# Optimization experiments

Measured on AMD Instinct MI355X. Metric: run time of the kernel, lower is better.

The kernel has to match this reference:

```python
import jax, jax.numpy as jnp
import numpy as np

L, B, N, D = 512, 8, 32, 256
GH, AH = 128, 64  # gate hidden, attn hidden


def setup_inputs() -> dict:
    key = jax.random.key(0)
    ks = jax.random.split(key, 11)
    s = lambda fan_in: 1.0 / np.sqrt(fan_in)
    return {
        "vert_feat": jax.random.normal(ks[0], (L, B, N, D), jnp.float32),
        "horiz_feat": jax.random.normal(ks[1], (L, B, N, D), jnp.float32),
        "mask_BNL": jax.random.bernoulli(ks[2], 0.5, (B, N, L)),
        "gw1": jax.random.uniform(ks[3], (GH, 2 * D), jnp.float32, -s(2 * D), s(2 * D)),
        "gb1": jax.random.uniform(ks[4], (GH,), jnp.float32, -s(2 * D), s(2 * D)),
        "gw2": jax.random.uniform(ks[5], (1, GH), jnp.float32, -s(GH), s(GH)),
        "gb2": jax.random.uniform(ks[6], (1,), jnp.float32, -s(GH), s(GH)),
        "aw1": jax.random.uniform(ks[7], (AH, D), jnp.float32, -s(D), s(D)),
        "ab1": jax.random.uniform(ks[8], (AH,), jnp.float32, -s(D), s(D)),
        "aw2": jax.random.uniform(ks[9], (1, AH), jnp.float32, -s(AH), s(AH)),
        "ab2": jax.random.uniform(ks[10], (1,), jnp.float32, -s(AH), s(AH)),
    }


def reference(vert_feat, horiz_feat, mask_BNL, gw1, gb1, gw2, gb2, aw1, ab1, aw2, ab2):
    # gate MLP on concat features: [L,B,N,2D] -> [L,B,N,1]
    comb = jnp.concatenate([vert_feat, horiz_feat], axis=-1)
    h = jax.nn.relu(comb @ gw1.T + gb1)
    gate = jax.nn.sigmoid(h @ gw2.T + gb2)  # [L,B,N,1]
    per_msg = gate * vert_feat + (1.0 - gate) * horiz_feat  # [L,B,N,D]
    # scorer MLP -> logits [L,B,N]
    a = jnp.tanh(per_msg @ aw1.T + ab1)
    logits = (a @ aw2.T + ab2)[..., 0]  # [L,B,N]
    logits_BLN = jnp.transpose(logits, (1, 0, 2))  # [B,L,N]
    mask_BLN = jnp.transpose(mask_BNL, (0, 2, 1))  # [B,L,N]
    logits_BLN = jnp.where(mask_BLN, logits_BLN, -jnp.inf)
    attn = jax.nn.softmax(logits_BLN, axis=-1)
    attn = jnp.nan_to_num(attn, nan=0.0)  # rows fully masked -> 0
    # weighted sum over messages: per_msg as [B,L,N,D]
    fused_BLD = jnp.einsum("bln,lbnd->bld", attn, per_msg)
    fused = jnp.transpose(fused_BLD, (1, 0, 2))  # [L,B,D]
    return fused, per_msg, attn
```

## Files before the change

### kernel.cpp

```cpp
#include <hip/hip_runtime.h>
#include <hip/hip_bf16.h>
#include <math.h>

#define LL 512
#define BB 8
#define NN 32
#define DD 256
#define GH 128
#define AH 64

#define PA 520

typedef short short8 __attribute__((ext_vector_type(8)));
typedef float f32x4  __attribute__((ext_vector_type(4)));

__device__ __forceinline__ float bf2f(unsigned short u) {
  return __uint_as_float(((unsigned int)u) << 16);
}
__device__ __forceinline__ unsigned short f2bf(float f) {
  union { __hip_bfloat16 h; unsigned short u; } cv;
  cv.h = __float2bfloat16(f);
  return cv.u;
}

extern "C" __global__ void wconv(const float* __restrict__ gw1,
                                 const float* __restrict__ aw1,
                                 unsigned short* __restrict__ ws)
{
  int o = blockIdx.x * 256 + threadIdx.x;
  if (o < 65536) {
    int kb = o >> 12, r = o & 4095, j = r >> 5, ko = r & 31;
    ws[o] = f2bf(gw1[j * 512 + kb * 32 + ko]);
  } else {
    int o2 = o - 65536;
    int kb = o2 >> 11, j = (o2 >> 5) & 63, ko = o2 & 31;
    ws[o] = f2bf(aw1[j * 256 + kb * 32 + ko]);
  }
}

extern "C" __global__ __launch_bounds__(256, 4)
void dynfusion_kernel(const float* __restrict__ vert,
                      const float* __restrict__ horiz,
                      const int*   __restrict__ mask,
                      const float* __restrict__ gb1,
                      const float* __restrict__ gw2,
                      const float* __restrict__ gb2,
                      const float* __restrict__ ab1,
                      const float* __restrict__ aw2,
                      const float* __restrict__ ab2,
                      const unsigned short* __restrict__ ws,
                      float* __restrict__ out)
{
  __shared__ __align__(16) unsigned short sA[NN * PA];
  __shared__ float sPart[NN][2];
  __shared__ float sGb1R[GH], sGw2R[GH];
  __shared__ float sAb1R[AH], sAw2R[AH];
  __shared__ float sGate[NN], sAttn[NN], sScal[2];

  const int t  = threadIdx.x;
  const int lb = blockIdx.x;
  const int l  = lb >> 3;
  const int b  = lb & 7;
  const size_t msgBase = (size_t)lb * NN * DD;

  const int lane = t & 63;
  const int w    = t >> 6;
  const int lr   = lane & 15;
  const int lg   = lane >> 4;
  const int mt   = w & 1;
  const int ns   = (w >> 1) << 6;
  const int js   = (w >> 1) << 5;
  const int aoff = (mt * 16 + lr) * PA;

  const unsigned short* __restrict__ gw1t = ws;
  const unsigned short* __restrict__ aw1t = ws + 65536;

  float* __restrict__ outF  = out;
  float* __restrict__ outPM = out + 1048576;
  float* __restrict__ outAT = out + 34603008;

  int mval = 0;
  if (t < NN) mval = mask[((size_t)b * NN + t) * LL + l];

  if (t < GH) { sGb1R[t] = gb1[t]; sGw2R[t] = gw2[t]; }
  if (t < AH) { sAb1R[t] = ab1[t]; sAw2R[t] = aw2[t]; }
  if (t == 0) { sScal[0] = gb2[0]; sScal[1] = ab2[0]; }

#pragma unroll
  for (int i = 0; i < 16; ++i) {
    int idx4 = i * 256 + t;
    int n  = idx4 >> 7;
    int c4 = (idx4 & 127) << 2;
    const float* src = (c4 < DD) ? (vert  + msgBase + n * DD + c4)
                                 : (horiz + msgBase + n * DD + (c4 - DD));
    float4 v4 = *reinterpret_cast<const float4*>(src);
    ushort4 pk;
    pk.x = f2bf(v4.x); pk.y = f2bf(v4.y); pk.z = f2bf(v4.z); pk.w = f2bf(v4.w);
    *reinterpret_cast<ushort4*>(&sA[n * PA + c4]) = pk;
  }
  __syncthreads();

  f32x4 acc1[4] = {};
  {
    const unsigned short* bgp = gw1t + (ns + lr) * 32 + lg * 8;
#pragma unroll
    for (int ks = 0; ks < 16; ++ks) {
      short8 af = *reinterpret_cast<const short8*>(&sA[aoff + ks * 32 + lg * 8]);
#pragma unroll
      for (int nt = 0; nt < 4; ++nt) {
        short8 bf = *reinterpret_cast<const short8*>(bgp + ks * 4096 + nt * 512);
        acc1[nt] = __builtin_amdgcn_mfma_f32_16x16x32_bf16(af, bf, acc1[nt], 0, 0, 0);
      }
    }
  }

  {
    float p[4] = {0.f, 0.f, 0.f, 0.f};
#pragma unroll
    for (int nt = 0; nt < 4; ++nt) {
      int j = ns + nt * 16 + lr;
      float bj = sGb1R[j], wj = sGw2R[j];
#pragma unroll
      for (int r = 0; r < 4; ++r) {
        float hv = fmaxf(acc1[nt][r] + bj, 0.0f);
        p[r] += hv * wj;
      }
    }
#pragma unroll
    for (int msk = 1; msk <= 8; msk <<= 1)
#pragma unroll
      for (int r = 0; r < 4; ++r) p[r] += __shfl_xor(p[r], msk);
    if (lr == 0) {
#pragma unroll
      for (int r = 0; r < 4; ++r) sPart[mt * 16 + lg * 4 + r][w >> 1] = p[r];
    }
  }
  __syncthreads();
  if (t < NN) {
    float sv = sScal[0] + sPart[t][0] + sPart[t][1];
    sGate[t] = 1.0f / (1.0f + __expf(-sv));
  }
  __syncthreads();

#pragma unroll
  for (int i = 0; i < 8; ++i) {
    int idx4 = i * 256 + t;
    int n  = idx4 >> 6;
    int d0 = (idx4 & 63) << 2;
    float g = sGate[n];
    ushort4 vq = *reinterpret_cast<const ushort4*>(&sA[n * PA + d0]);
    ushort4 hq = *reinterpret_cast<const ushort4*>(&sA[n * PA + DD + d0]);
    float4 pr;
    pr.x = bf2f(hq.x) + g * (bf2f(vq.x) - bf2f(hq.x));
    pr.y = bf2f(hq.y) + g * (bf2f(vq.y) - bf2f(hq.y));
    pr.z = bf2f(hq.z) + g * (bf2f(vq.z) - bf2f(hq.z));
    pr.w = bf2f(hq.w) + g * (bf2f(vq.w) - bf2f(hq.w));
    ushort4 pq;
    pq.x = f2bf(pr.x); pq.y = f2bf(pr.y); pq.z = f2bf(pr.z); pq.w = f2bf(pr.w);
    *reinterpret_cast<ushort4*>(&sA[n * PA + d0]) = pq;
    *reinterpret_cast<float4*>(outPM + msgBase + n * DD + d0) = pr;
  }
  __syncthreads();

  f32x4 acc2[2] = {};
  {
    const unsigned short* bap = aw1t + (js + lr) * 32 + lg * 8;
#pragma unroll
    for (int ks = 0; ks < 8; ++ks) {
      short8 af = *reinterpret_cast<const short8*>(&sA[aoff + ks * 32 + lg * 8]);
#pragma unroll
      for (int q = 0; q < 2; ++q) {
        short8 bf = *reinterpret_cast<const short8*>(bap + ks * 2048 + q * 512);
        acc2[q] = __builtin_amdgcn_mfma_f32_16x16x32_bf16(af, bf, acc2[q], 0, 0, 0);
      }
    }
  }

  {
    float p[4] = {0.f, 0.f, 0.f, 0.f};
#pragma unroll
    for (int q = 0; q < 2; ++q) {
      int j = js + q * 16 + lr;
      float bj = sAb1R[j], wj = sAw2R[j];
#pragma unroll
      for (int r = 0; r < 4; ++r) {
        float av = tanhf(acc2[q][r] + bj);
        p[r] += av * wj;
      }
    }
#pragma unroll
    for (int msk = 1; msk <= 8; msk <<= 1)
#pragma unroll
      for (int r = 0; r < 4; ++r) p[r] += __shfl_xor(p[r], msk);
    if (lr == 0) {
#pragma unroll
      for (int r = 0; r < 4; ++r) sPart[mt * 16 + lg * 4 + r][w >> 1] = p[r];
    }
  }
  __syncthreads();

  if (t < 64) {
    float logit = -INFINITY;
    bool valid = false;
    if (t < 32) {
      float sv = sScal[1] + sPart[t][0] + sPart[t][1];
      valid = (mval != 0);
      logit = valid ? sv : -INFINITY;
    }
    float m = logit;
#pragma unroll
    for (int off = 32; off >= 1; off >>= 1) m = fmaxf(m, __shfl_xor(m, off));
    float e = (valid && m > -INFINITY) ? __expf(logit - m) : 0.0f;
    float ssum = e;
#pragma unroll
    for (int off = 32; off >= 1; off >>= 1) ssum += __shfl_xor(ssum, off);
    float at = (ssum > 0.0f) ? (e / ssum) : 0.0f;
    if (t < 32) {
      sAttn[t] = at;
      outAT[((size_t)b * LL + l) * NN + t] = at;
    }
  }
  __syncthreads();

  {
    int d = t;
    float f = 0.0f;
#pragma unroll
    for (int n = 0; n < NN; ++n) f += sAttn[n] * bf2f(sA[n * PA + d]);
    outF[(size_t)lb * DD + d] = f;
  }
}

extern "C" void kernel_launch(void* const* d_in, const int* in_sizes, int n_in,
                              void* d_out, int out_size, void* d_ws, size_t ws_size,
                              hipStream_t stream) {
  wconv<<<dim3(320), dim3(256), 0, stream>>>(
      (const float*)d_in[3],
      (const float*)d_in[7],
      (unsigned short*)d_ws);

  dynfusion_kernel<<<dim3(LL * BB), dim3(256), 0, stream>>>(
      (const float*)d_in[0],
      (const float*)d_in[1],
      (const int*)d_in[2],
      (const float*)d_in[4],
      (const float*)d_in[5],
      (const float*)d_in[6],
      (const float*)d_in[8],
      (const float*)d_in[9],
      (const float*)d_in[10],
      (const unsigned short*)d_ws,
      (float*)d_out);
}
```

Before: 389.2 us.

## Process four (l,b) groups per block with register-prefetched next inputs

Each block now loops over four consecutive (l,b) groups. The next group's vert/horiz tile and mask are loaded into registers while the current group's MFMA and softmax stages run, so global-load latency overlaps compute. The change also swaps __syncthreads for a barrier that waits only on LDS counters, and raises wave priority around the MFMA loops. The cost is 64 extra float registers per thread for the prefetch, which may cut occupancy, plus a grid four times smaller.

```diff
diff --git a/kernel.cpp b/kernel.cpp
--- a/kernel.cpp
+++ b/kernel.cpp
@@ -10,6 +10,8 @@
 #define AH 64
 
 #define PA 520
+#define NPAIR 4
+#define NBLK (LL * BB / NPAIR)
 
 typedef short short8 __attribute__((ext_vector_type(8)));
 typedef float f32x4  __attribute__((ext_vector_type(4)));
@@ -21,6 +23,12 @@
   union { __hip_bfloat16 h; unsigned short u; } cv;
   cv.h = __float2bfloat16(f);
   return cv.u;
+}
+
+__device__ __forceinline__ void barrier_lds() {
+  asm volatile("s_waitcnt lgkmcnt(0)" ::: "memory");
+  __builtin_amdgcn_s_barrier();
+  __builtin_amdgcn_sched_barrier(0);
 }
 
 extern "C" __global__ void wconv(const float* __restrict__ gw1,
@@ -57,11 +65,8 @@
   __shared__ float sAb1R[AH], sAw2R[AH];
   __shared__ float sGate[NN], sAttn[NN], sScal[2];
 
-  const int t  = threadIdx.x;
-  const int lb = blockIdx.x;
-  const int l  = lb >> 3;
-  const int b  = lb & 7;
-  const size_t msgBase = (size_t)lb * NN * DD;
+  const int t   = threadIdx.x;
+  const int bid = blockIdx.x;
 
   const int lane = t & 63;
   const int w    = t >> 6;
@@ -79,155 +84,202 @@
   float* __restrict__ outPM = out + 1048576;
   float* __restrict__ outAT = out + 34603008;
 
-  int mval = 0;
-  if (t < NN) mval = mask[((size_t)b * NN + t) * LL + l];
-
   if (t < GH) { sGb1R[t] = gb1[t]; sGw2R[t] = gw2[t]; }
   if (t < AH) { sAb1R[t] = ab1[t]; sAw2R[t] = aw2[t]; }
   if (t == 0) { sScal[0] = gb2[0]; sScal[1] = ab2[0]; }
 
-#pragma unroll
-  for (int i = 0; i < 16; ++i) {
-    int idx4 = i * 256 + t;
-    int n  = idx4 >> 7;
-    int c4 = (idx4 & 127) << 2;
-    const float* src = (c4 < DD) ? (vert  + msgBase + n * DD + c4)
-                                 : (horiz + msgBase + n * DD + (c4 - DD));
-    float4 v4 = *reinterpret_cast<const float4*>(src);
-    ushort4 pk;
-    pk.x = f2bf(v4.x); pk.y = f2bf(v4.y); pk.z = f2bf(v4.z); pk.w = f2bf(v4.w);
-    *reinterpret_cast<ushort4*>(&sA[n * PA + c4]) = pk;
+  float4 pf[16];
+  {
+    const size_t base0 = (size_t)(bid * NPAIR) * NN * DD;
+#pragma unroll
+    for (int i = 0; i < 16; ++i) {
+      int idx4 = i * 256 + t;
+      int n  = idx4 >> 7;
+      int c4 = (idx4 & 127) << 2;
+      const float* src = (c4 < DD) ? (vert  + base0 + n * DD + c4)
+                                   : (horiz + base0 + n * DD + (c4 - DD));
+      pf[i] = *reinterpret_cast<const float4*>(src);
+    }
   }
-  __syncthreads();
-
-  f32x4 acc1[4] = {};
+  int mval = 0;
   {
-    const unsigned short* bgp = gw1t + (ns + lr) * 32 + lg * 8;
-#pragma unroll
-    for (int ks = 0; ks < 16; ++ks) {
-      short8 af = *reinterpret_cast<const short8*>(&sA[aoff + ks * 32 + lg * 8]);
+    int lb0 = bid * NPAIR;
+    if (t < NN) mval = mask[((size_t)(lb0 & 7) * NN + t) * LL + (lb0 >> 3)];
+  }
+
+#pragma unroll 1
+  for (int p = 0; p < NPAIR; ++p) {
+    const int lb = bid * NPAIR + p;
+    const int l  = lb >> 3;
+    const int b  = lb & 7;
+    const size_t msgBase = (size_t)lb * NN * DD;
+
+    __syncthreads();
+
+#pragma unroll
+    for (int i = 0; i < 16; ++i) {
+      int idx4 = i * 256 + t;
+      int n  = idx4 >> 7;
+      int c4 = (idx4 & 127) << 2;
+      ushort4 pk;
+      pk.x = f2bf(pf[i].x); pk.y = f2bf(pf[i].y);
+      pk.z = f2bf(pf[i].z); pk.w = f2bf(pf[i].w);
+      *reinterpret_cast<ushort4*>(&sA[n * PA + c4]) = pk;
+    }
+
+    int mnext = 0;
+    if (p + 1 < NPAIR) {
+      const size_t baseN = msgBase + (size_t)NN * DD;
+#pragma unroll
+      for (int i = 0; i < 16; ++i) {
+        int idx4 = i * 256 + t;
+        int n  = idx4 >> 7;
+        int c4 = (idx4 & 127) << 2;
+        const float* src = (c4 < DD) ? (vert  + baseN + n * DD + c4)
+                                     : (horiz + baseN + n * DD + (c4 - DD));
+        pf[i] = *reinterpret_cast<const float4*>(src);
+      }
+      int lb2 = lb + 1;
+      if (t < NN) mnext = mask[((size_t)(lb2 & 7) * NN + t) * LL + (lb2 >> 3)];
+    }
+
+    barrier_lds();
+
+    f32x4 acc1[4] = {};
+    {
+      const unsigned short* bgp = gw1t + (ns + lr) * 32 + lg * 8;
+      __builtin_amdgcn_s_setprio(1);
+#pragma unroll
+      for (int ks = 0; ks < 16; ++ks) {
+        short8 af = *reinterpret_cast<const short8*>(&sA[aoff + ks * 32 + lg * 8]);
+#pragma unroll
+        for (int nt = 0; nt < 4; ++nt) {
+          short8 bf = *reinterpret_cast<const short8*>(bgp + ks * 4096 + nt * 512);
+          acc1[nt] = __builtin_amdgcn_mfma_f32_16x16x32_bf16(af, bf, acc1[nt], 0, 0, 0);
+        }
+      }
+      __builtin_amdgcn_s_setprio(0);
+    }
+
+    {
+      float pr[4] = {0.f, 0.f, 0.f, 0.f};
 #pragma unroll
       for (int nt = 0; nt < 4; ++nt) {
-        short8 bf = *reinterpret_cast<const short8*>(bgp + ks * 4096 + nt * 512);
-        acc1[nt] = __builtin_amdgcn_mfma_f32_16x16x32_bf16(af, bf, acc1[nt], 0, 0, 0);
-      }
-    }
-  }
-
-  {
-    float p[4] = {0.f, 0.f, 0.f, 0.f};
-#pragma unroll
-    for (int nt = 0; nt < 4; ++nt) {
-      int j = ns + nt * 16 + lr;
-      float bj = sGb1R[j], wj = sGw2R[j];
-#pragma unroll
-      for (int r = 0; r < 4; ++r) {
-        float hv = fmaxf(acc1[nt][r] + bj, 0.0f);
-        p[r] += hv * wj;
-      }
-    }
-#pragma unroll
-    for (int msk = 1; msk <= 8; msk <<= 1)
-#pragma unroll
-      for (int r = 0; r < 4; ++r) p[r] += __shfl_xor(p[r], msk);
-    if (lr == 0) {
-#pragma unroll
-      for (int r = 0; r < 4; ++r) sPart[mt * 16 + lg * 4 + r][w >> 1] = p[r];
-    }
-  }
-  __syncthreads();
-  if (t < NN) {
-    float sv = sScal[0] + sPart[t][0] + sPart[t][1];
-    sGate[t] = 1.0f / (1.0f + __expf(-sv));
-  }
-  __syncthreads();
-
-#pragma unroll
-  for (int i = 0; i < 8; ++i) {
-    int idx4 = i * 256 + t;
-    int n  = idx4 >> 6;
-    int d0 = (idx4 & 63) << 2;
-    float g = sGate[n];
-    ushort4 vq = *reinterpret_cast<const ushort4*>(&sA[n * PA + d0]);
-    ushort4 hq = *reinterpret_cast<const ushort4*>(&sA[n * PA + DD + d0]);
-    float4 pr;
-    pr.x = bf2f(hq.x) + g * (bf2f(vq.x) - bf2f(hq.x));
-    pr.y = bf2f(hq.y) + g * (bf2f(vq.y) - bf2f(hq.y));
-    pr.z = bf2f(hq.z) + g * (bf2f(vq.z) - bf2f(hq.z));
-    pr.w = bf2f(hq.w) + g * (bf2f(vq.w) - bf2f(hq.w));
-    ushort4 pq;
-    pq.x = f2bf(pr.x); pq.y = f2bf(pr.y); pq.z = f2bf(pr.z); pq.w = f2bf(pr.w);
-    *reinterpret_cast<ushort4*>(&sA[n * PA + d0]) = pq;
-    *reinterpret_cast<float4*>(outPM + msgBase + n * DD + d0) = pr;
-  }
-  __syncthreads();
-
-  f32x4 acc2[2] = {};
-  {
-    const unsigned short* bap = aw1t + (js + lr) * 32 + lg * 8;
-#pragma unroll
-    for (int ks = 0; ks < 8; ++ks) {
-      short8 af = *reinterpret_cast<const short8*>(&sA[aoff + ks * 32 + lg * 8]);
+        int j = ns + nt * 16 + lr;
+        float bj = sGb1R[j], wj = sGw2R[j];
+#pragma unroll
+        for (int r = 0; r < 4; ++r) {
+          float hv = fmaxf(acc1[nt][r] + bj, 0.0f);
+          pr[r] += hv * wj;
+        }
+      }
+#pragma unroll
+      for (int msk = 1; msk <= 8; msk <<= 1)
+#pragma unroll
+        for (int r = 0; r < 4; ++r) pr[r] += __shfl_xor(pr[r], msk);
+      if (lr == 0) {
+#pragma unroll
+        for (int r = 0; r < 4; ++r) sPart[mt * 16 + lg * 4 + r][w >> 1] = pr[r];
+      }
+    }
+    barrier_lds();
+    if (t < NN) {
+      float sv = sScal[0] + sPart[t][0] + sPart[t][1];
+      sGate[t] = 1.0f / (1.0f + __expf(-sv));
+    }
+    barrier_lds();
+
+#pragma unroll
+    for (int i = 0; i < 8; ++i) {
+      int idx4 = i * 256 + t;
+      int n  = idx4 >> 6;
+      int d0 = (idx4 & 63) << 2;
+      float g = sGate[n];
+      ushort4 vq = *reinterpret_cast<const ushort4*>(&sA[n * PA + d0]);
+      ushort4 hq = *reinterpret_cast<const ushort4*>(&sA[n * PA + DD + d0]);
+      float4 prv;
+      prv.x = bf2f(hq.x) + g * (bf2f(vq.x) - bf2f(hq.x));
+      prv.y = bf2f(hq.y) + g * (bf2f(vq.y) - bf2f(hq.y));
+      prv.z = bf2f(hq.z) + g * (bf2f(vq.z) - bf2f(hq.z));
+      prv.w = bf2f(hq.w) + g * (bf2f(vq.w) - bf2f(hq.w));
+      ushort4 pq;
+      pq.x = f2bf(prv.x); pq.y = f2bf(prv.y); pq.z = f2bf(prv.z); pq.w = f2bf(prv.w);
+      *reinterpret_cast<ushort4*>(&sA[n * PA + d0]) = pq;
+      *reinterpret_cast<float4*>(outPM + msgBase + n * DD + d0) = prv;
+    }
+    barrier_lds();
+
+    f32x4 acc2[2] = {};
+    {
+      const unsigned short* bap = aw1t + (js + lr) * 32 + lg * 8;
+      __builtin_amdgcn_s_setprio(1);
+#pragma unroll
+      for (int ks = 0; ks < 8; ++ks) {
+        short8 af = *reinterpret_cast<const short8*>(&sA[aoff + ks * 32 + lg * 8]);
+#pragma unroll
+        for (int q = 0; q < 2; ++q) {
+          short8 bf = *reinterpret_cast<const short8*>(bap + ks * 2048 + q * 512);
+          acc2[q] = __builtin_amdgcn_mfma_f32_16x16x32_bf16(af, bf, acc2[q], 0, 0, 0);
+        }
+      }
+      __builtin_amdgcn_s_setprio(0);
+    }
+
+    {
+      float pr[4] = {0.f, 0.f, 0.f, 0.f};
 #pragma unroll
       for (int q = 0; q < 2; ++q) {
-        short8 bf = *reinterpret_cast<const short8*>(bap + ks * 2048 + q * 512);
-        acc2[q] = __builtin_amdgcn_mfma_f32_16x16x32_bf16(af, bf, acc2[q], 0, 0, 0);
-      }
-    }
-  }
-
-  {
-    float p[4] = {0.f, 0.f, 0.f, 0.f};
-#pragma unroll
-    for (int q = 0; q < 2; ++q) {
-      int j = js + q * 16 + lr;
-      float bj = sAb1R[j], wj = sAw2R[j];
-#pragma unroll
-      for (int r = 0; r < 4; ++r) {
-        float av = tanhf(acc2[q][r] + bj);
-        p[r] += av * wj;
-      }
-    }
-#pragma unroll
-    for (int msk = 1; msk <= 8; msk <<= 1)
-#pragma unroll
-      for (int r = 0; r < 4; ++r) p[r] += __shfl_xor(p[r], msk);
-    if (lr == 0) {
-#pragma unroll
-      for (int r = 0; r < 4; ++r) sPart[mt * 16 + lg * 4 + r][w >> 1] = p[r];
-    }
-  }
-  __syncthreads();
-
-  if (t < 64) {
-    float logit = -INFINITY;
-    bool valid = false;
-    if (t < 32) {
-      float sv = sScal[1] + sPart[t][0] + sPart[t][1];
-      valid = (mval != 0);
-      logit = valid ? sv : -INFINITY;
-    }
-    float m = logit;
-#pragma unroll
-    for (int off = 32; off >= 1; off >>= 1) m = fmaxf(m, __shfl_xor(m, off));
-    float e = (valid && m > -INFINITY) ? __expf(logit - m) : 0.0f;
-    float ssum = e;
-#pragma unroll
-    for (int off = 32; off >= 1; off >>= 1) ssum += __shfl_xor(ssum, off);
-    float at = (ssum > 0.0f) ? (e / ssum) : 0.0f;
-    if (t < 32) {
-      sAttn[t] = at;
-      outAT[((size_t)b * LL + l) * NN + t] = at;
-    }
-  }
-  __syncthreads();
-
-  {
-    int d = t;
-    float f = 0.0f;
-#pragma unroll
-    for (int n = 0; n < NN; ++n) f += sAttn[n] * bf2f(sA[n * PA + d]);
-    outF[(size_t)lb * DD + d] = f;
+        int j = js + q * 16 + lr;
+        float bj = sAb1R[j], wj = sAw2R[j];
+#pragma unroll
+        for (int r = 0; r < 4; ++r) {
+          float av = tanhf(acc2[q][r] + bj);
+          pr[r] += av * wj;
+        }
+      }
+#pragma unroll
+      for (int msk = 1; msk <= 8; msk <<= 1)
+#pragma unroll
+        for (int r = 0; r < 4; ++r) pr[r] += __shfl_xor(pr[r], msk);
+      if (lr == 0) {
+#pragma unroll
+        for (int r = 0; r < 4; ++r) sPart[mt * 16 + lg * 4 + r][w >> 1] = pr[r];
+      }
+    }
+    barrier_lds();
+
+    if (t < 64) {
+      float logit = -INFINITY;
+      bool valid = false;
+      if (t < 32) {
+        float sv = sScal[1] + sPart[t][0] + sPart[t][1];
+        valid = (mval != 0);
+        logit = valid ? sv : -INFINITY;
+      }
+      float m = logit;
+#pragma unroll
+      for (int off = 32; off >= 1; off >>= 1) m = fmaxf(m, __shfl_xor(m, off));
+      float e = (valid && m > -INFINITY) ? __expf(logit - m) : 0.0f;
+      float ssum = e;
+#pragma unroll
+      for (int off = 32; off >= 1; off >>= 1) ssum += __shfl_xor(ssum, off);
+      float at = (ssum > 0.0f) ? (e / ssum) : 0.0f;
+      if (t < 32) {
+        sAttn[t] = at;
+        outAT[((size_t)b * LL + l) * NN + t] = at;
+      }
+    }
+    barrier_lds();
+
+    {
+      int d = t;
+      float f = 0.0f;
+#pragma unroll
+      for (int n = 0; n < NN; ++n) f += sAttn[n] * bf2f(sA[n * PA + d]);
+      outF[(size_t)lb * DD + d] = f;
+    }
+
+    mval = mnext;
   }
 }
 
@@ -239,7 +291,7 @@
       (const float*)d_in[7],
       (unsigned short*)d_ws);
 
-  dynfusion_kernel<<<dim3(LL * BB), dim3(256), 0, stream>>>(
+  dynfusion_kernel<<<dim3(NBLK), dim3(256), 0, stream>>>(
       (const float*)d_in[0],
       (const float*)d_in[1],
       (const int*)d_in[2],
```

Result: slower. 632.5 us (+62.5%).
